# Kernel tuning notes

Hardware: AMD Instinct MI355X
Metric: run time of the kernel (lower is better)

## Reference

```python
import jax, jax.numpy as jnp
import numpy as np

EPS = 1e-07
N, Q = 1368, 21
WS = [16, 32, 64]
ST = [4, 8, 16]
OC = [64, 128, 256]


def _num_pos(n, w, s):
    return int((n - w) / s - EPS) + 1


def setup_inputs() -> dict:
    key = jax.random.key(0)
    kx, k0, k1, k2 = jax.random.split(key, 4)
    B = 64
    x = jax.random.normal(kx, (B, Q, N), dtype=jnp.float32)
    ws = []
    for kk, (w, s, d) in zip([k0, k1, k2], zip(WS, ST, OC)):
        P = _num_pos(N, w, s)
        # xavier-style small init, shape (Nk, q*w) as in FilterbankLinear.weight
        scale = np.sqrt(2.0 / (Q * w + d)).astype(np.float32)
        ws.append(scale * jax.random.normal(kk, (d * P, Q * w), dtype=jnp.float32))
    return {"x": x, "w0": ws[0], "w1": ws[1], "w2": ws[2]}


def _filterbank_linear(x, W, w, s, d):
    # x: (B, q, N); W: (d*P, q*w)
    B, q, n = x.shape
    P = _num_pos(n, w, s)
    # window starts: j*s for j in range(P-1), last window anchored at n-w
    starts = np.concatenate([np.arange(P - 1) * s, np.array([n - w])])
    idx = starts[:, None] + np.arange(w)            # (P, w) static gather indices
    win = x[:, :, idx]                              # (B, q, P, w)
    win = jnp.transpose(win, (0, 2, 1, 3)).reshape(B, P, q * w)  # (B, P, q*w), channel-major like fbank
    h = jnp.einsum('bpf,pdf->bpd', win, W.reshape(P, d, q * w))
    return h.reshape(B, P * d)


def reference(x, w0, w1, w2):
    # FilterbankEdge.forward(x, sample=False): concat of each FilterbankLinear output
    outs = [
        _filterbank_linear(x, W, w, s, d)
        for W, (w, s, d) in zip([w0, w1, w2], zip(WS, ST, OC))
    ]
    return jnp.concatenate(outs, axis=-1)  # (B, 64000)
```

## Files before the change

kernel.cpp:

```cpp
#include <hip/hip_runtime.h>

#define QDIM 21
#define NDIM 1368
#define OUTSTRIDE 64000

typedef __attribute__((ext_vector_type(4))) float f32x4;
typedef __attribute__((ext_vector_type(8))) short bf16x8s;
typedef __attribute__((ext_vector_type(4))) unsigned int u32x4;

typedef __attribute__((address_space(1))) const unsigned int* gas_p;
typedef __attribute__((address_space(3))) unsigned int* las_p;

static __device__ __forceinline__ void gload16(const float* g, char* l) {
    __builtin_amdgcn_global_load_lds((gas_p)(const void*)g, (las_p)(void*)l, 16, 0, 0);
}

static __device__ __forceinline__ unsigned int pk2(float lo, float hi) {
    unsigned int a = __float_as_uint(lo) + 0x8000u;
    unsigned int b = __float_as_uint(hi) + 0x8000u;
    return __builtin_amdgcn_perm(b, a, 0x07060302);
}

static __device__ __forceinline__ bf16x8s pack8(f32x4 lo, f32x4 hi) {
    u32x4 p;
    p[0] = pk2(lo[0], lo[1]);
    p[1] = pk2(lo[2], lo[3]);
    p[2] = pk2(hi[0], hi[1]);
    p[3] = pk2(hi[2], hi[3]);
    return __builtin_bit_cast(bf16x8s, p);
}

template<int WLOG2, int NTX, int D, int P, int S, int K>
__device__ __forceinline__ void fbk_body(const float* __restrict__ x,
                                         const float* __restrict__ W,
                                         float* __restrict__ out, int bid,
                                         char* ldsraw) {
    constexpr int WWIN = 1 << WLOG2;
    constexpr int G = (K + 31) / 32;
    constexpr bool TAIL = (K % 32) != 0;
    constexpr int FMAXC = (K - 4) & ~3;

    const int n0 = (bid % NTX) * 64;
    const int p  = bid / NTX;
    const int start = (p == P - 1) ? (NDIM - WWIN) : p * S;

    const int tid  = threadIdx.x;
    const int wid  = tid >> 6;
    const int lane = tid & 63;
    const int wm = (wid >> 1) * 32;
    const int wn = (wid & 1) * 32;
    const int lr = lane & 15;
    const int hi = lane >> 4;
    const int kb = hi * 8;

    const int lrow = lane >> 3;
    const int g4   = ((lane & 7) ^ lrow) * 4;
    const int r0   = 16 * wid + lrow;
    const float* xb0 = x + (size_t)r0 * QDIM * NDIM + start;
    const float* Wp  = W + (size_t)(p * D + n0) * K;
    const float* wb0 = Wp + (size_t)r0 * K;
    const float* wb1 = wb0 + (size_t)8 * K;
    const int wA = 2048 * wid;

    auto STAGE = [&](int t, int sbase) {
        int f = t * 32 + g4;
        if constexpr (TAIL) f = (f > FMAXC) ? FMAXC : f;
        int q = f >> WLOG2;
        int j = f & (WWIN - 1);
        const float* ga = xb0 + q * NDIM + j;
        char* la = ldsraw + sbase + wA;
        char* lb = ldsraw + sbase + 8192 + wA;
        gload16(ga, la);
        gload16(ga + (size_t)8 * QDIM * NDIM, la + 1024);
        gload16(wb0 + f, lb);
        gload16(wb1 + f, lb + 1024);
    };

    const int x7 = lr & 7;
    const int c0 = ((hi * 2)     ^ x7) * 16;
    const int c1 = ((hi * 2 + 1) ^ x7) * 16;
    const int oA0 = (wm + lr) * 128;
    const int oA1 = (wm + 16 + lr) * 128;
    const int oB0 = 8192 + (wn + lr) * 128;
    const int oB1 = 8192 + (wn + 16 + lr) * 128;

    f32x4 acc[2][2] = {};

    STAGE(0, 0);
    STAGE(1, 16384);

    int cs = 0;
    #pragma unroll 1
    for (int t = 0; t < G; ++t) {
        if (t + 1 < G) { asm volatile("s_waitcnt vmcnt(4)" ::: "memory"); }
        else           { asm volatile("s_waitcnt vmcnt(0)" ::: "memory"); }
        __builtin_amdgcn_sched_barrier(0);
        __builtin_amdgcn_s_barrier();
        __builtin_amdgcn_sched_barrier(0);

        const char* sb = ldsraw + cs;
        f32x4 a00 = *(const f32x4*)(sb + oA0 + c0);
        f32x4 a01 = *(const f32x4*)(sb + oA0 + c1);
        f32x4 a10 = *(const f32x4*)(sb + oA1 + c0);
        f32x4 a11 = *(const f32x4*)(sb + oA1 + c1);
        f32x4 b00 = *(const f32x4*)(sb + oB0 + c0);
        f32x4 b01 = *(const f32x4*)(sb + oB0 + c1);
        f32x4 b10 = *(const f32x4*)(sb + oB1 + c0);
        f32x4 b11 = *(const f32x4*)(sb + oB1 + c1);

        if constexpr (TAIL) {
            if (t == G - 1 && kb >= (K & 31)) {
                f32x4 z = {0.f, 0.f, 0.f, 0.f};
                a00 = z; a01 = z; a10 = z; a11 = z;
            }
        }

        bf16x8s A0 = pack8(a00, a01);
        bf16x8s A1 = pack8(a10, a11);
        bf16x8s B0 = pack8(b00, b01);
        bf16x8s B1 = pack8(b10, b11);

        acc[0][0] = __builtin_amdgcn_mfma_f32_16x16x32_bf16(A0, B0, acc[0][0], 0, 0, 0);
        acc[0][1] = __builtin_amdgcn_mfma_f32_16x16x32_bf16(A0, B1, acc[0][1], 0, 0, 0);
        acc[1][0] = __builtin_amdgcn_mfma_f32_16x16x32_bf16(A1, B0, acc[1][0], 0, 0, 0);
        acc[1][1] = __builtin_amdgcn_mfma_f32_16x16x32_bf16(A1, B1, acc[1][1], 0, 0, 0);

        __builtin_amdgcn_sched_barrier(0);
        if (t + 2 < G) {
            int pb = (cs == 0) ? 32768 : cs - 16384;
            STAGE(t + 2, pb);
        }
        cs = (cs == 32768) ? 0 : cs + 16384;
    }

    const int colbase = p * D + n0;
    #pragma unroll
    for (int mi = 0; mi < 2; ++mi) {
        #pragma unroll
        for (int ni = 0; ni < 2; ++ni) {
            int col = colbase + wn + ni * 16 + lr;
            int rbase = wm + mi * 16 + hi * 4;
            #pragma unroll
            for (int r = 0; r < 4; ++r) {
                out[(size_t)(rbase + r) * OUTSTRIDE + col] = acc[mi][ni][r];
            }
        }
    }
}

__global__ __launch_bounds__(256, 3)
void fbk_fused(const float* __restrict__ x,  const float* __restrict__ w0,
               const float* __restrict__ w1, const float* __restrict__ w2,
               float* __restrict__ out) {
    __shared__ __align__(16) char ldsraw[49152];
    const int k = blockIdx.x & 7;
    const int i = blockIdx.x >> 3;
    int seg, r;
    if (i < 123)      { seg = i % 3;              r = i / 3;  }
    else if (k < 6)   { seg = (i == 123) ? 1 : 2; r = 41;     }
    else              { seg = 2;                  r = i - 82; }
    if (seg == 0) {
        fbk_body<6, 4, 256, 82, 16, 1344>(x, w2, out + 43008, 41 * k + r, ldsraw);
    } else if (seg == 1) {
        int base = (k < 7) ? 42 * k : 293;
        fbk_body<5, 2, 128, 167, 8, 672>(x, w1, out + 21632, base + r, ldsraw);
    } else {
        int base = (k < 7) ? 42 * k : 295;
        fbk_body<4, 1, 64, 338, 4, 336>(x, w0, out, base + r, ldsraw);
    }
}

extern "C" void kernel_launch(void* const* d_in, const int* in_sizes, int n_in,
                              void* d_out, int out_size, void* d_ws, size_t ws_size,
                              hipStream_t stream) {
    const float* x  = (const float*)d_in[0];
    const float* w0 = (const float*)d_in[1];
    const float* w1 = (const float*)d_in[2];
    const float* w2 = (const float*)d_in[3];
    float* out = (float*)d_out;
    fbk_fused<<<dim3(1000), 256, 0, stream>>>(x, w0, w1, w2, out);
}
```

Measured before the change: 45.43 us.

## Pre-convert x to bf16 in a workspace pass and restructure LDS pipeline

Adds a separate kernel that converts x to bf16 in the workspace so the main GEMM kernel loads half as many A bytes and skips in-loop packing for A. The LDS ring is resized (3-stage with smaller A tiles for the bf16 path, 2-stage otherwise), occupancy is raised to 4 blocks per CU, and block-to-work mapping is changed to contiguous chunks per XCD. The extra conversion launch adds a full read and write of x plus launch overhead, and the fp32 fallback path now uses a shallower double buffer.

```diff
diff --git a/kernel.cpp b/kernel.cpp
--- a/kernel.cpp
+++ b/kernel.cpp
@@ -3,6 +3,7 @@
 #define QDIM 21
 #define NDIM 1368
 #define OUTSTRIDE 64000
+#define XTOT (64 * QDIM * NDIM)
 
 typedef __attribute__((ext_vector_type(4))) float f32x4;
 typedef __attribute__((ext_vector_type(8))) short bf16x8s;
@@ -11,8 +12,8 @@
 typedef __attribute__((address_space(1))) const unsigned int* gas_p;
 typedef __attribute__((address_space(3))) unsigned int* las_p;
 
-static __device__ __forceinline__ void gload16(const float* g, char* l) {
-    __builtin_amdgcn_global_load_lds((gas_p)(const void*)g, (las_p)(void*)l, 16, 0, 0);
+static __device__ __forceinline__ void gload16(const void* g, char* l) {
+    __builtin_amdgcn_global_load_lds((gas_p)g, (las_p)(void*)l, 16, 0, 0);
 }
 
 static __device__ __forceinline__ unsigned int pk2(float lo, float hi) {
@@ -30,8 +31,26 @@
     return __builtin_bit_cast(bf16x8s, p);
 }
 
-template<int WLOG2, int NTX, int D, int P, int S, int K>
+static __device__ __forceinline__ int chunk_swz(int idx, int n) {
+    int xcd = idx & 7;
+    int i   = idx >> 3;
+    int q = n >> 3, r = n & 7;
+    int base = (xcd < r) ? xcd * (q + 1) : r * (q + 1) + (xcd - r) * q;
+    return base + i;
+}
+
+__global__ __launch_bounds__(256)
+void xcvt(const float* __restrict__ x, unsigned short* __restrict__ xb) {
+    int i = (blockIdx.x * 256 + threadIdx.x) * 8;
+    if (i >= XTOT) return;
+    f32x4 lo = *(const f32x4*)(x + i);
+    f32x4 hi = *(const f32x4*)(x + i + 4);
+    *(u32x4*)(xb + i) = __builtin_bit_cast(u32x4, pack8(lo, hi));
+}
+
+template<int WLOG2, int NTX, int D, int P, int S, int K, bool ABF16>
 __device__ __forceinline__ void fbk_body(const float* __restrict__ x,
+                                         const unsigned short* __restrict__ xb,
                                          const float* __restrict__ W,
                                          float* __restrict__ out, int bid,
                                          char* ldsraw) {
@@ -39,6 +58,9 @@
     constexpr int G = (K + 31) / 32;
     constexpr bool TAIL = (K % 32) != 0;
     constexpr int FMAXC = (K - 4) & ~3;
+    constexpr int ASTB = ABF16 ? 4096 : 8192;
+    constexpr int STB  = ASTB + 8192;
+    constexpr int RING = ABF16 ? 3 : 2;
 
     const int n0 = (bid % NTX) * 64;
     const int p  = bid / NTX;
@@ -55,23 +77,36 @@
 
     const int lrow = lane >> 3;
     const int g4   = ((lane & 7) ^ lrow) * 4;
-    const int r0   = 16 * wid + lrow;
-    const float* xb0 = x + (size_t)r0 * QDIM * NDIM + start;
     const float* Wp  = W + (size_t)(p * D + n0) * K;
-    const float* wb0 = Wp + (size_t)r0 * K;
+    const float* wb0 = Wp + (size_t)(16 * wid + lrow) * K;
     const float* wb1 = wb0 + (size_t)8 * K;
-    const int wA = 2048 * wid;
+    const int wB = 2048 * wid;
+
+    const unsigned short* xbrow = nullptr;
+    if constexpr (ABF16)
+        xbrow = xb + (size_t)(16 * wid + (lane >> 2)) * (QDIM * NDIM) + start;
+    const float* xb0f = x + (size_t)(16 * wid + lrow) * (QDIM * NDIM) + start;
+    const int wA = ABF16 ? (1024 * wid) : (2048 * wid);
 
     auto STAGE = [&](int t, int sbase) {
+        if constexpr (ABF16) {
+            int f = t * 32 + (lane & 3) * 8;
+            int q = f >> WLOG2;
+            int j = f & (WWIN - 1);
+            gload16(xbrow + q * NDIM + j, ldsraw + sbase + wA);
+        } else {
+            int f = t * 32 + g4;
+            if constexpr (TAIL) f = (f > FMAXC) ? FMAXC : f;
+            int q = f >> WLOG2;
+            int j = f & (WWIN - 1);
+            const float* ga = xb0f + q * NDIM + j;
+            char* la = ldsraw + sbase + wA;
+            gload16(ga, la);
+            gload16(ga + (size_t)8 * QDIM * NDIM, la + 1024);
+        }
         int f = t * 32 + g4;
         if constexpr (TAIL) f = (f > FMAXC) ? FMAXC : f;
-        int q = f >> WLOG2;
-        int j = f & (WWIN - 1);
-        const float* ga = xb0 + q * NDIM + j;
-        char* la = ldsraw + sbase + wA;
-        char* lb = ldsraw + sbase + 8192 + wA;
-        gload16(ga, la);
-        gload16(ga + (size_t)8 * QDIM * NDIM, la + 1024);
+        char* lb = ldsraw + sbase + ASTB + wB;
         gload16(wb0 + f, lb);
         gload16(wb1 + f, lb + 1024);
     };
@@ -79,44 +114,59 @@
     const int x7 = lr & 7;
     const int c0 = ((hi * 2)     ^ x7) * 16;
     const int c1 = ((hi * 2 + 1) ^ x7) * 16;
+    const int oA0b = (wm + lr) * 64 + hi * 16;
+    const int oA1b = oA0b + 1024;
     const int oA0 = (wm + lr) * 128;
     const int oA1 = (wm + 16 + lr) * 128;
-    const int oB0 = 8192 + (wn + lr) * 128;
-    const int oB1 = 8192 + (wn + 16 + lr) * 128;
+    const int oB0 = ASTB + (wn + lr) * 128;
+    const int oB1 = ASTB + (wn + 16 + lr) * 128;
 
     f32x4 acc[2][2] = {};
 
     STAGE(0, 0);
-    STAGE(1, 16384);
+    if constexpr (RING == 3) STAGE(1, STB);
 
     int cs = 0;
     #pragma unroll 1
     for (int t = 0; t < G; ++t) {
-        if (t + 1 < G) { asm volatile("s_waitcnt vmcnt(4)" ::: "memory"); }
-        else           { asm volatile("s_waitcnt vmcnt(0)" ::: "memory"); }
+        if constexpr (RING == 3) {
+            if (t + 1 < G) { asm volatile("s_waitcnt vmcnt(3)" ::: "memory"); }
+            else           { asm volatile("s_waitcnt vmcnt(0)" ::: "memory"); }
+        } else {
+            asm volatile("s_waitcnt vmcnt(0)" ::: "memory");
+        }
         __builtin_amdgcn_sched_barrier(0);
         __builtin_amdgcn_s_barrier();
         __builtin_amdgcn_sched_barrier(0);
 
+        if constexpr (RING == 2) {
+            if (t + 1 < G) STAGE(t + 1, cs ^ STB);
+            __builtin_amdgcn_sched_barrier(0);
+        }
+
         const char* sb = ldsraw + cs;
-        f32x4 a00 = *(const f32x4*)(sb + oA0 + c0);
-        f32x4 a01 = *(const f32x4*)(sb + oA0 + c1);
-        f32x4 a10 = *(const f32x4*)(sb + oA1 + c0);
-        f32x4 a11 = *(const f32x4*)(sb + oA1 + c1);
+        bf16x8s A0, A1;
+        if constexpr (ABF16) {
+            A0 = *(const bf16x8s*)(sb + oA0b);
+            A1 = *(const bf16x8s*)(sb + oA1b);
+        } else {
+            f32x4 a00 = *(const f32x4*)(sb + oA0 + c0);
+            f32x4 a01 = *(const f32x4*)(sb + oA0 + c1);
+            f32x4 a10 = *(const f32x4*)(sb + oA1 + c0);
+            f32x4 a11 = *(const f32x4*)(sb + oA1 + c1);
+            if constexpr (TAIL) {
+                if (t == G - 1 && kb >= (K & 31)) {
+                    f32x4 z = {0.f, 0.f, 0.f, 0.f};
+                    a00 = z; a01 = z; a10 = z; a11 = z;
+                }
+            }
+            A0 = pack8(a00, a01);
+            A1 = pack8(a10, a11);
+        }
         f32x4 b00 = *(const f32x4*)(sb + oB0 + c0);
         f32x4 b01 = *(const f32x4*)(sb + oB0 + c1);
         f32x4 b10 = *(const f32x4*)(sb + oB1 + c0);
         f32x4 b11 = *(const f32x4*)(sb + oB1 + c1);
-
-        if constexpr (TAIL) {
-            if (t == G - 1 && kb >= (K & 31)) {
-                f32x4 z = {0.f, 0.f, 0.f, 0.f};
-                a00 = z; a01 = z; a10 = z; a11 = z;
-            }
-        }
-
-        bf16x8s A0 = pack8(a00, a01);
-        bf16x8s A1 = pack8(a10, a11);
         bf16x8s B0 = pack8(b00, b01);
         bf16x8s B1 = pack8(b10, b11);
 
@@ -126,11 +176,15 @@
         acc[1][1] = __builtin_amdgcn_mfma_f32_16x16x32_bf16(A1, B1, acc[1][1], 0, 0, 0);
 
         __builtin_amdgcn_sched_barrier(0);
-        if (t + 2 < G) {
-            int pb = (cs == 0) ? 32768 : cs - 16384;
-            STAGE(t + 2, pb);
-        }
-        cs = (cs == 32768) ? 0 : cs + 16384;
+        if constexpr (RING == 3) {
+            if (t + 2 < G) {
+                int pb = (cs == 0) ? 2 * STB : cs - STB;
+                STAGE(t + 2, pb);
+            }
+            cs = (cs == 2 * STB) ? 0 : cs + STB;
+        } else {
+            cs ^= STB;
+        }
     }
 
     const int colbase = p * D + n0;
@@ -148,25 +202,19 @@
     }
 }
 
-__global__ __launch_bounds__(256, 3)
-void fbk_fused(const float* __restrict__ x,  const float* __restrict__ w0,
-               const float* __restrict__ w1, const float* __restrict__ w2,
-               float* __restrict__ out) {
-    __shared__ __align__(16) char ldsraw[49152];
-    const int k = blockIdx.x & 7;
-    const int i = blockIdx.x >> 3;
-    int seg, r;
-    if (i < 123)      { seg = i % 3;              r = i / 3;  }
-    else if (k < 6)   { seg = (i == 123) ? 1 : 2; r = 41;     }
-    else              { seg = 2;                  r = i - 82; }
-    if (seg == 0) {
-        fbk_body<6, 4, 256, 82, 16, 1344>(x, w2, out + 43008, 41 * k + r, ldsraw);
-    } else if (seg == 1) {
-        int base = (k < 7) ? 42 * k : 293;
-        fbk_body<5, 2, 128, 167, 8, 672>(x, w1, out + 21632, base + r, ldsraw);
+template<bool BF>
+__global__ __launch_bounds__(256, 4)
+void fbk_fused(const float* __restrict__ x,  const unsigned short* __restrict__ xb,
+               const float* __restrict__ w0, const float* __restrict__ w1,
+               const float* __restrict__ w2, float* __restrict__ out) {
+    __shared__ __align__(16) char ldsraw[36864];
+    const int pb = blockIdx.x;
+    if (pb < 328) {
+        fbk_body<6, 4, 256, 82, 16, 1344, BF>(x, xb, w2, out + 43008, chunk_swz(pb, 328), ldsraw);
+    } else if (pb < 662) {
+        fbk_body<5, 2, 128, 167, 8, 672, BF>(x, xb, w1, out + 21632, chunk_swz(pb - 328, 334), ldsraw);
     } else {
-        int base = (k < 7) ? 42 * k : 295;
-        fbk_body<4, 1, 64, 338, 4, 336>(x, w0, out, base + r, ldsraw);
+        fbk_body<4, 1, 64, 338, 4, 336, false>(x, xb, w0, out, chunk_swz(pb - 662, 338), ldsraw);
     }
 }
 
@@ -178,5 +226,12 @@
     const float* w1 = (const float*)d_in[2];
     const float* w2 = (const float*)d_in[3];
     float* out = (float*)d_out;
-    fbk_fused<<<dim3(1000), 256, 0, stream>>>(x, w0, w1, w2, out);
-}
+    constexpr size_t XBF_BYTES = (size_t)XTOT * 2;
+    if (ws_size >= XBF_BYTES) {
+        unsigned short* xbuf = (unsigned short*)d_ws;
+        xcvt<<<dim3((XTOT / 8 + 255) / 256), 256, 0, stream>>>(x, xbuf);
+        fbk_fused<true><<<dim3(1000), 256, 0, stream>>>(x, xbuf, w0, w1, w2, out);
+    } else {
+        fbk_fused<false><<<dim3(1000), 256, 0, stream>>>(x, nullptr, w0, w1, w2, out);
+    }
+}
```

Measured after the change: 45.56 us. About the same (+0.3%).
